# Performance work log

Measured on AMD Instinct MI355X. Metric: run time of the kernel, lower is better.

The kernel has to match this reference:

```python
import jax, jax.numpy as jnp
import numpy as np

N, E, IN, H, OUT, K = 50000, 800000, 128, 128, 40, 10
ALPHA, EPS, AH = 0.1, 1e-5, 64


def setup_inputs() -> dict:
    key = jax.random.key(0)
    ks = jax.random.split(key, 32)
    rn = lambda k, s, sc=0.05: jax.random.normal(k, s, jnp.float32) * sc
    return dict(
        x=jax.random.normal(ks[0], (N, IN), jnp.float32),
        edge_index=jax.random.randint(ks[1], (2, E), 0, N, jnp.int64),
        edge_weight=jax.random.uniform(ks[2], (E,), jnp.float32),
        lin1_w=rn(ks[3], (H, IN)), lin1_b=rn(ks[4], (H,)),
        bn1_g=jnp.ones((H,), jnp.float32), bn1_b=jnp.zeros((H,), jnp.float32),
        bn1_m=rn(ks[5], (H,)), bn1_v=jax.random.uniform(ks[6], (H,), jnp.float32, 0.5, 1.5),
        lin2_w=rn(ks[7], (H, H)), lin2_b=rn(ks[8], (H,)),
        bn2_g=jnp.ones((H,), jnp.float32), bn2_b=jnp.zeros((H,), jnp.float32),
        bn2_m=rn(ks[9], (H,)), bn2_v=jax.random.uniform(ks[10], (H,), jnp.float32, 0.5, 1.5),
        att1_w=rn(ks[11], (AH, 2 * H)), att1_b=rn(ks[12], (AH,)),
        att2_w=rn(ks[13], (K + 1, AH)), att2_b=rn(ks[14], (K + 1,)),
        head1_w=rn(ks[15], (H // 2, H)), head1_b=rn(ks[16], (H // 2,)),
        bn3_g=jnp.ones((H // 2,), jnp.float32), bn3_b=jnp.zeros((H // 2,), jnp.float32),
        bn3_m=rn(ks[17], (H // 2,)), bn3_v=jax.random.uniform(ks[18], (H // 2,), jnp.float32, 0.5, 1.5),
        head2_w=rn(ks[19], (OUT, H // 2)), head2_b=rn(ks[20], (OUT,)),
    )


def _bn(x, g, b, m, v):
    # eval-mode BatchNorm1d with running stats
    return (x - m) * jax.lax.rsqrt(v + EPS) * g + b


def reference(x, edge_index, edge_weight,
              lin1_w, lin1_b, bn1_g, bn1_b, bn1_m, bn1_v,
              lin2_w, lin2_b, bn2_g, bn2_b, bn2_m, bn2_v,
              att1_w, att1_b, att2_w, att2_b,
              head1_w, head1_b, bn3_g, bn3_b, bn3_m, bn3_v,
              head2_w, head2_b):
    row, col = edge_index[0], edge_index[1]

    # dense stem (dropout is identity in eval mode)
    h = jax.nn.relu(_bn(x @ lin1_w.T + lin1_b, bn1_g, bn1_b, bn1_m, bn1_v))
    identity = h
    h = jax.nn.relu(_bn(h @ lin2_w.T + lin2_b, bn2_g, bn2_b, bn2_m, bn2_v)) + identity
    base = h  # h0 for APPNP

    # edge normalization (loop-invariant): w_e / clamp(sum_w(row), 1)
    wsum = jnp.clip(jax.ops.segment_sum(edge_weight, row, num_segments=N), 1.0)
    enorm = edge_weight / wsum[row]  # [E]

    xs = [h]
    for _ in range(K):  # fixed K iterations of gather -> scatter-add
        agg = jax.ops.segment_sum(h[row] * enorm[:, None], col, num_segments=N)
        h = (1.0 - ALPHA) * agg + ALPHA * base
        xs.append(h)

    stacked = jnp.stack(xs, axis=-1)                    # [N, H, K+1]
    ctx = jnp.concatenate([xs[0], xs[-1]], axis=-1)     # [N, 2H]
    a = jax.nn.gelu(ctx @ att1_w.T + att1_b, approximate=False) @ att2_w.T + att2_b
    w = jax.nn.softmax(a, axis=-1)[:, None, :]          # [N, 1, K+1]
    fused = (stacked * w).sum(axis=-1)                  # [N, H]

    z = jax.nn.relu(_bn(fused @ head1_w.T + head1_b, bn3_g, bn3_b, bn3_m, bn3_v))
    return z @ head2_w.T + head2_b
```

## Files before the change

### kernel.cpp

```cpp
#include <hip/hip_runtime.h>
#include <hip/hip_fp16.h>
#include <math.h>

#define NN 50000
#define EE 800000
#define HH 128
#define KIT 10
#define NHF (NN * HH)
#define CC 64
#define CH 12500
#define RRH 4
#define NRH 12500

typedef _Float16 half8 __attribute__((ext_vector_type(8)));
typedef _Float16 half4v __attribute__((ext_vector_type(4)));
typedef float floatx4 __attribute__((ext_vector_type(4)));

static_assert(NN % 16 == 0, "row tiles must be exact");

__device__ __forceinline__ float gelu_exact(float x) {
  return 0.5f * x * (1.f + erff(x * 0.70710678118654752f));
}

__device__ __forceinline__ float4 ld4(const float* p) { return *(const float4*)p; }
__device__ __forceinline__ float4 ld4(const __half* p) {
  const __half2* q = (const __half2*)p;
  float2 lo = __half22float2(q[0]);
  float2 hi = __half22float2(q[1]);
  return make_float4(lo.x, lo.y, hi.x, hi.y);
}
__device__ __forceinline__ void st1(float* p, float v) { *p = v; }
__device__ __forceinline__ void st1(__half* p, float v) { *p = __float2half_rn(v); }

__global__ __launch_bounds__(256) void hist2_kernel(const int* __restrict__ ei,
                                                    const float* __restrict__ ew,
                                                    int* __restrict__ pdeg,
                                                    float* __restrict__ pwsum,
                                                    int* __restrict__ rank) {
  __shared__ int hist[NRH];
  const int c = blockIdx.x;
  const int z = blockIdx.y;
  const bool isdeg = (z < RRH);
  const int lo = (isdeg ? z : z - RRH) * NRH;
  for (int i = threadIdx.x; i < NRH; i += 256) hist[i] = 0;
  __syncthreads();
  const int e0 = c * CH;
  if (isdeg) {
    const int4* d4 = (const int4*)(ei + (size_t)EE + e0);
    for (int i = threadIdx.x; i < CH / 4; i += 256) {
      int4 d = d4[i];
      int e = e0 + i * 4;
      unsigned u0 = (unsigned)(d.x - lo), u1 = (unsigned)(d.y - lo);
      unsigned u2 = (unsigned)(d.z - lo), u3 = (unsigned)(d.w - lo);
      if (u0 < NRH) rank[e]     = atomicAdd(&hist[u0], 1);
      if (u1 < NRH) rank[e + 1] = atomicAdd(&hist[u1], 1);
      if (u2 < NRH) rank[e + 2] = atomicAdd(&hist[u2], 1);
      if (u3 < NRH) rank[e + 3] = atomicAdd(&hist[u3], 1);
    }
    __syncthreads();
    for (int i = threadIdx.x; i < NRH; i += 256)
      pdeg[(size_t)c * NN + lo + i] = hist[i];
  } else {
    float* whist = (float*)hist;
    const int4* s4 = (const int4*)(ei + e0);
    const float4* w4 = (const float4*)(ew + e0);
    for (int i = threadIdx.x; i < CH / 4; i += 256) {
      int4 s = s4[i];
      float4 w = w4[i];
      unsigned u0 = (unsigned)(s.x - lo), u1 = (unsigned)(s.y - lo);
      unsigned u2 = (unsigned)(s.z - lo), u3 = (unsigned)(s.w - lo);
      if (u0 < NRH) atomicAdd(&whist[u0], w.x);
      if (u1 < NRH) atomicAdd(&whist[u1], w.y);
      if (u2 < NRH) atomicAdd(&whist[u2], w.z);
      if (u3 < NRH) atomicAdd(&whist[u3], w.w);
    }
    __syncthreads();
    for (int i = threadIdx.x; i < NRH; i += 256)
      pwsum[(size_t)c * NN + lo + i] = whist[i];
  }
}

__global__ __launch_bounds__(256) void reduce_kernel(int* __restrict__ pdeg,
                                                     const float* __restrict__ pwsum,
                                                     int* __restrict__ deg,
                                                     float* __restrict__ wsum,
                                                     int* __restrict__ bsum) {
  int node = blockIdx.x * 256 + threadIdx.x;
  int acc = 0; float wacc = 0.f;
  if (node < NN) {
    for (int c = 0; c < CC; ++c) {
      size_t idx = (size_t)c * NN + node;
      int t = pdeg[idx];
      pdeg[idx] = acc;
      acc += t;
      wacc += pwsum[idx];
    }
    deg[node] = acc;
    wsum[node] = wacc;
  }
  __shared__ int red[256];
  red[threadIdx.x] = (node < NN) ? ((acc + 7) & ~7) : 0;
  __syncthreads();
  for (int off = 128; off > 0; off >>= 1) {
    if (threadIdx.x < off) red[threadIdx.x] += red[threadIdx.x + off];
    __syncthreads();
  }
  if (threadIdx.x == 0) bsum[blockIdx.x] = red[0];
}

__global__ __launch_bounds__(256) void scan2_kernel(const int* __restrict__ bsum,
                                                    int* __restrict__ boff,
                                                    int* __restrict__ row_start, int nb, int n) {
  __shared__ int buf[256];
  int tid = threadIdx.x;
  int v = (tid < nb) ? bsum[tid] : 0;
  buf[tid] = v;
  __syncthreads();
  for (int off = 1; off < 256; off <<= 1) {
    int t = (tid >= off) ? buf[tid - off] : 0;
    __syncthreads();
    buf[tid] += t;
    __syncthreads();
  }
  if (tid < nb) boff[tid] = buf[tid] - v;
  if (tid == 255) row_start[n] = buf[255];
}

__global__ __launch_bounds__(256) void scan3_kernel(const int* __restrict__ deg,
                                                    const int* __restrict__ boff,
                                                    int* __restrict__ row_start, int n) {
  __shared__ int buf[256];
  int tid = threadIdx.x;
  int i = blockIdx.x * 256 + tid;
  int v = (i < n) ? ((deg[i] + 7) & ~7) : 0;
  buf[tid] = v;
  __syncthreads();
  for (int off = 1; off < 256; off <<= 1) {
    int t = (tid >= off) ? buf[tid - off] : 0;
    __syncthreads();
    buf[tid] += t;
    __syncthreads();
  }
  if (i < n) row_start[i] = boff[blockIdx.x] + buf[tid] - v;
}

__global__ __launch_bounds__(256) void csr_fill_kernel(const int* __restrict__ ei,
                                                       const float* __restrict__ ew,
                                                       const float* __restrict__ wsum,
                                                       const int* __restrict__ row_start,
                                                       const int* __restrict__ pdeg_excl,
                                                       const int* __restrict__ rank,
                                                       int2* __restrict__ csr, int e_cnt) {
  int e = blockIdx.x * 256 + threadIdx.x;
  if (e >= e_cnt) return;
  int c = e / CH;
  int src = ei[e], dst = ei[EE + e];
  float ws = wsum[src];
  ws = ws < 1.f ? 1.f : ws;
  float v = 0.9f * ew[e] / ws;
  int pos = row_start[dst] + pdeg_excl[(size_t)c * NN + dst] + rank[e];
  csr[pos] = make_int2(src, __float_as_int(v));
}

__global__ __launch_bounds__(256) void pad_fill_kernel(const int* __restrict__ deg,
                                                       const int* __restrict__ row_start,
                                                       long* __restrict__ csr) {
  int node = blockIdx.x * 256 + threadIdx.x;
  if (node >= NN) return;
  int s = row_start[node] + deg[node];
  int e = row_start[node + 1];
  for (int i = s; i < e; ++i) csr[i] = 0;
}

__global__ __launch_bounds__(256, 6) void prop_kernel(const __half* __restrict__ h_cur,
                                                      const __half* __restrict__ base,
                                                      const int* __restrict__ row_start,
                                                      const long* __restrict__ csr,
                                                      __half* __restrict__ h_next) {
  int pair = __builtin_amdgcn_readfirstlane((int)blockIdx.x * 4 + (int)(threadIdx.x >> 6));
  int nA = pair * 2;
  if (nA >= NN) return;
  int nB = nA + 1;
  int lane = threadIdx.x & 63;
  const __half2* hc = (const __half2*)h_cur;
  float2 vbA = __half22float2(((const __half2*)base)[(size_t)nA * 64 + lane]);
  float2 vbB = __half22float2(((const __half2*)base)[(size_t)nB * 64 + lane]);
  float aAx = 0.1f * vbA.x, aAy = 0.1f * vbA.y, bAx = 0.f, bAy = 0.f;
  float aBx = 0.1f * vbB.x, aBy = 0.1f * vbB.y, bBx = 0.f, bBy = 0.f;
  int s  = __builtin_amdgcn_readfirstlane(row_start[nA]);
  int eA = __builtin_amdgcn_readfirstlane(row_start[nA + 1]);
  int eB = __builtin_amdgcn_readfirstlane(row_start[nB + 1]);
  int nb = (eB - s) >> 3;
  int i = s;
  if (nb > 0) {
    long cur[8];
    bool curB = (i >= eA);
#pragma unroll
    for (int j = 0; j < 8; ++j) cur[j] = csr[i + j];
    i += 8;
    for (int bidx = 1; bidx < nb; ++bidx) {
      long nxt[8];
      bool nxtB = (i >= eA);
#pragma unroll
      for (int j = 0; j < 8; ++j) nxt[j] = csr[i + j];
      i += 8;
      float2 g[8];
#pragma unroll
      for (int j = 0; j < 8; ++j) g[j] = __half22float2(hc[(size_t)(int)cur[j] * 64 + lane]);
      if (curB) {
#pragma unroll
        for (int j = 0; j < 8; ++j) {
          float v = __int_as_float((int)(cur[j] >> 32));
          if (j & 1) { bBx = fmaf(v, g[j].x, bBx); bBy = fmaf(v, g[j].y, bBy); }
          else       { aBx = fmaf(v, g[j].x, aBx); aBy = fmaf(v, g[j].y, aBy); }
        }
      } else {
#pragma unroll
        for (int j = 0; j < 8; ++j) {
          float v = __int_as_float((int)(cur[j] >> 32));
          if (j & 1) { bAx = fmaf(v, g[j].x, bAx); bAy = fmaf(v, g[j].y, bAy); }
          else       { aAx = fmaf(v, g[j].x, aAx); aAy = fmaf(v, g[j].y, aAy); }
        }
      }
#pragma unroll
      for (int j = 0; j < 8; ++j) cur[j] = nxt[j];
      curB = nxtB;
    }
    float2 g[8];
#pragma unroll
    for (int j = 0; j < 8; ++j) g[j] = __half22float2(hc[(size_t)(int)cur[j] * 64 + lane]);
    if (curB) {
#pragma unroll
      for (int j = 0; j < 8; ++j) {
        float v = __int_as_float((int)(cur[j] >> 32));
        if (j & 1) { bBx = fmaf(v, g[j].x, bBx); bBy = fmaf(v, g[j].y, bBy); }
        else       { aBx = fmaf(v, g[j].x, aBx); aBy = fmaf(v, g[j].y, aBy); }
      }
    } else {
#pragma unroll
      for (int j = 0; j < 8; ++j) {
        float v = __int_as_float((int)(cur[j] >> 32));
        if (j & 1) { bAx = fmaf(v, g[j].x, bAx); bAy = fmaf(v, g[j].y, bAy); }
        else       { aAx = fmaf(v, g[j].x, aAx); aAy = fmaf(v, g[j].y, aAy); }
      }
    }
  }
  ((__half2*)h_next)[(size_t)nA * 64 + lane] =
      __float22half2_rn(make_float2(aAx + bAx, aAy + bAy));
  ((__half2*)h_next)[(size_t)nB * 64 + lane] =
      __float22half2_rn(make_float2(aBx + bBx, aBy + bBy));
}

template <int K, int KA, int JP, int JR, int ACT, bool RESID, typename IT, typename OT>
__global__ __launch_bounds__(256) void mfma_dense2(
    const IT* __restrict__ Xa, const IT* __restrict__ Xb,
    const float* __restrict__ W, const float* __restrict__ lb,
    const float* __restrict__ bg, const float* __restrict__ bb,
    const float* __restrict__ bm, const float* __restrict__ bv,
    const OT* __restrict__ resid, OT* __restrict__ out) {
  static_assert(K % 32 == 0 && KA % 32 == 0 && JP % 16 == 0, "");
  constexpr int JT = JP / 16;
  constexpr int NS = K / 32;
  constexpr bool ISF = __is_same(IT, float);
  __shared__ _Float16 wL[JP][K];

  const int tid = threadIdx.x;
  const int wv = tid >> 6, lane = tid & 63;
  const int q = lane >> 4, m = lane & 15;
  const int t = blockIdx.x * 4 + wv;
  const bool active = (t < NN / 16);
  const int row = t * 16 + m;

  half8  a[ISF ? 1 : NS];
  float4 af0[ISF ? NS : 1], af1[ISF ? NS : 1];
  if (active) {
#pragma unroll
    for (int s = 0; s < NS; ++s) {
      int c = s * 32 + q * 8;
      if constexpr (ISF) {
        const float* p = (const float*)Xa + (size_t)row * K + c;
        af0[s] = *(const float4*)p;
        af1[s] = *(const float4*)(p + 4);
      } else {
        const __half* p = (c < KA) ? (const __half*)Xa + (size_t)row * KA + c
                                   : (const __half*)Xb + (size_t)row * (K - KA) + (c - KA);
        a[s] = *(const half8*)p;
      }
    }
  }

  constexpr int C4 = K / 4;
  for (int idx = tid; idx < JP * C4; idx += 256) {
    int j = idx / C4;
    int c4 = (idx % C4) * 4;
    float4 v = make_float4(0.f, 0.f, 0.f, 0.f);
    if (j < JR) v = *(const float4*)&W[(size_t)j * K + c4];
    int cs = ((((c4 >> 3) ^ (j & 7)) << 3) | (c4 & 7));
    *(half4v*)&wL[j][cs] = (half4v){(_Float16)v.x, (_Float16)v.y,
                                    (_Float16)v.z, (_Float16)v.w};
  }
  __syncthreads();

  if (!active) return;

  floatx4 acc[JT];
#pragma unroll
  for (int jt = 0; jt < JT; ++jt) acc[jt] = (floatx4)(0.f);

#pragma unroll
  for (int s = 0; s < NS; ++s) {
    half8 av;
    if constexpr (ISF) {
      float4 f0 = af0[s], f1 = af1[s];
      av = (half8){(_Float16)f0.x, (_Float16)f0.y, (_Float16)f0.z, (_Float16)f0.w,
                   (_Float16)f1.x, (_Float16)f1.y, (_Float16)f1.z, (_Float16)f1.w};
    } else {
      av = a[s];
    }
    int kq = s * 4 + q;
#pragma unroll
    for (int jt = 0; jt < JT; ++jt) {
      int j = jt * 16 + m;
      half8 b = *(const half8*)&wL[j][(kq ^ (j & 7)) << 3];
      acc[jt] = __builtin_amdgcn_mfma_f32_16x16x32_f16(av, b, acc[jt], 0, 0, 0);
    }
  }

#pragma unroll
  for (int jt = 0; jt < JT; ++jt) {
    int j = jt * 16 + m;
    if (j >= JR) continue;
    float sc = 0.f, sh;
    if (ACT == 1) {
      sc = bg[j] * rsqrtf(bv[j] + 1e-5f);
      sh = (lb[j] - bm[j]) * sc + bb[j];
    } else {
      sh = lb[j];
    }
#pragma unroll
    for (int reg = 0; reg < 4; ++reg) {
      int r = t * 16 + q * 4 + reg;
      float aa = acc[jt][reg];
      float y;
      if (ACT == 0)      y = aa + sh;
      else if (ACT == 1) y = fmaxf(fmaf(aa, sc, sh), 0.f);
      else               y = gelu_exact(aa + sh);
      if (RESID) y += (float)resid[(size_t)r * JR + j];
      st1(&out[(size_t)r * JR + j], y);
    }
  }
}

__global__ __launch_bounds__(64) void att2_softmax_kernel(const __half* __restrict__ g,
                                                          const float* __restrict__ W2,
                                                          const float* __restrict__ b2,
                                                          float* __restrict__ attw, int n_rows) {
  __shared__ float gl[64][65];
  int r0 = blockIdx.x * 64;
  for (int idx = threadIdx.x; idx < 64 * 16; idx += 64) {
    int r = idx >> 4, c4 = (idx & 15) * 4;
    float4 v = make_float4(0.f, 0.f, 0.f, 0.f);
    if (r0 + r < n_rows) v = ld4(&g[(size_t)(r0 + r) * 64 + c4]);
    gl[r][c4] = v.x; gl[r][c4 + 1] = v.y; gl[r][c4 + 2] = v.z; gl[r][c4 + 3] = v.w;
  }
  __syncthreads();
  int r = threadIdx.x;
  int n = r0 + r;
  if (n >= n_rows) return;
  float a[KIT + 1];
#pragma unroll
  for (int j = 0; j < KIT + 1; ++j) {
    float acc = b2[j];
#pragma unroll
    for (int k = 0; k < 64; ++k) acc = fmaf(gl[r][k], W2[j * 64 + k], acc);
    a[j] = acc;
  }
  float mx = a[0];
#pragma unroll
  for (int j = 1; j < KIT + 1; ++j) mx = fmaxf(mx, a[j]);
  float s = 0.f;
#pragma unroll
  for (int j = 0; j < KIT + 1; ++j) { a[j] = expf(a[j] - mx); s += a[j]; }
  float inv = 1.f / s;
#pragma unroll
  for (int j = 0; j < KIT + 1; ++j) attw[n * 16 + j] = a[j] * inv;
}

__global__ __launch_bounds__(256) void fused_gather_kernel(const __half* __restrict__ XS,
                                                           const float* __restrict__ attw,
                                                           __half* __restrict__ fused) {
  int node = __builtin_amdgcn_readfirstlane((int)blockIdx.x * 4 + (int)(threadIdx.x >> 6));
  if (node >= NN) return;
  int lane = threadIdx.x & 63;
  float ax = 0.f, ay = 0.f;
#pragma unroll
  for (int k = 0; k <= KIT; ++k) {
    float wk = attw[node * 16 + k];
    float2 v = __half22float2(((const __half2*)(XS + (size_t)k * NHF))[(size_t)node * 64 + lane]);
    ax = fmaf(wk, v.x, ax);
    ay = fmaf(wk, v.y, ay);
  }
  ((__half2*)fused)[(size_t)node * 64 + lane] = __float22half2_rn(make_float2(ax, ay));
}

__global__ __launch_bounds__(256) void fused_accum_kernel(const __half* __restrict__ h,
                                                          const float* __restrict__ attw,
                                                          float* __restrict__ fused, int k) {
  int node = __builtin_amdgcn_readfirstlane((int)blockIdx.x * 4 + (int)(threadIdx.x >> 6));
  if (node >= NN) return;
  int lane = threadIdx.x & 63;
  float wk = attw[node * 16 + k];
  float2 v = __half22float2(((const __half2*)h)[(size_t)node * 64 + lane]);
  float2 o;
  if (k == 0) {
    o = make_float2(wk * v.x, wk * v.y);
  } else {
    float2 f = ((const float2*)fused)[(size_t)node * 64 + lane];
    o = make_float2(fmaf(wk, v.x, f.x), fmaf(wk, v.y, f.y));
  }
  ((float2*)fused)[(size_t)node * 64 + lane] = o;
}

extern "C" void kernel_launch(void* const* d_in, const int* in_sizes, int n_in,
                              void* d_out, int out_size, void* d_ws, size_t ws_size,
                              hipStream_t stream) {
  (void)in_sizes; (void)n_in; (void)out_size;
  const float* x      = (const float*)d_in[0];
  const int*   ei     = (const int*)d_in[1];
  const float* ew     = (const float*)d_in[2];
  const float* lin1_w = (const float*)d_in[3];
  const float* lin1_b = (const float*)d_in[4];
  const float* bn1_g  = (const float*)d_in[5];
  const float* bn1_b  = (const float*)d_in[6];
  const float* bn1_m  = (const float*)d_in[7];
  const float* bn1_v  = (const float*)d_in[8];
  const float* lin2_w = (const float*)d_in[9];
  const float* lin2_b = (const float*)d_in[10];
  const float* bn2_g  = (const float*)d_in[11];
  const float* bn2_b  = (const float*)d_in[12];
  const float* bn2_m  = (const float*)d_in[13];
  const float* bn2_v  = (const float*)d_in[14];
  const float* att1_w = (const float*)d_in[15];
  const float* att1_b = (const float*)d_in[16];
  const float* att2_w = (const float*)d_in[17];
  const float* att2_b = (const float*)d_in[18];
  const float* head1_w= (const float*)d_in[19];
  const float* head1_b= (const float*)d_in[20];
  const float* bn3_g  = (const float*)d_in[21];
  const float* bn3_b  = (const float*)d_in[22];
  const float* bn3_m  = (const float*)d_in[23];
  const float* bn3_v  = (const float*)d_in[24];
  const float* head2_w= (const float*)d_in[25];
  const float* head2_b= (const float*)d_in[26];
  float* out = (float*)d_out;

  char* p = (char*)d_ws;
  auto alloc = [&](size_t bytes) -> void* {
    void* r = (void*)p;
    p += (bytes + 255) & ~(size_t)255;
    return r;
  };
  int*   row_start= (int*)alloc((size_t)(NN + 1) * 4);
  int*   bsum     = (int*)alloc((size_t)256 * 4);
  int*   boff     = (int*)alloc((size_t)256 * 4);
  int*   deg      = (int*)alloc((size_t)NN * 4);
  float* wsum     = (float*)alloc((size_t)NN * 4);
  long*  csr      = (long*)alloc(((size_t)EE + 8 * NN) * 8);
  __half* gbuf    = (__half*)alloc((size_t)NN * 64 * 2);
  float* attw     = (float*)alloc((size_t)NN * 16 * 4);
  __half* h1      = (__half*)alloc((size_t)NHF * 2);
  __half* fusedH  = (__half*)alloc((size_t)NHF * 2);
  __half* zbuf    = (__half*)alloc((size_t)NN * 64 * 2);
  size_t common = (size_t)(p - (char*)d_ws);
  size_t stored_need = common + (size_t)(KIT + 1) * NHF * 2 + 4096;
  bool stored = ws_size >= stored_need;

  __half* XS = nullptr;
  int* pdeg; float* pwsum; int* rank;
  if (stored) {
    XS = (__half*)alloc((size_t)(KIT + 1) * NHF * 2);
    char* ovl = (char*)(XS + (size_t)8 * NHF);
    pdeg  = (int*)ovl;
    pwsum = (float*)(ovl + (size_t)CC * NN * 4);
    rank  = (int*)(ovl + 2 * (size_t)CC * NN * 4);
  } else {
    pdeg  = (int*)alloc((size_t)CC * NN * 4);
    pwsum = (float*)alloc((size_t)CC * NN * 4);
    rank  = (int*)alloc((size_t)EE * 4);
  }

  const int GE  = (EE + 255) / 256;
  const int GN  = (NN + 255) / 256;
  const int GT  = (NN / 16 + 3) / 4;
  const int GP  = (NN + 3) / 4;
  const int GP2 = (NN / 2 + 3) / 4;
  const int GA  = (NN + 63) / 64;

  hist2_kernel<<<dim3(CC, 2 * RRH), 256, 0, stream>>>(ei, ew, pdeg, pwsum, rank);
  reduce_kernel<<<GN, 256, 0, stream>>>(pdeg, pwsum, deg, wsum, bsum);
  scan2_kernel<<<1, 256, 0, stream>>>(bsum, boff, row_start, GN, NN);
  scan3_kernel<<<GN, 256, 0, stream>>>(deg, boff, row_start, NN);
  csr_fill_kernel<<<GE, 256, 0, stream>>>(ei, ew, wsum, row_start, pdeg, rank,
                                          (int2*)csr, EE);
  pad_fill_kernel<<<GN, 256, 0, stream>>>(deg, row_start, csr);

  if (stored) {
    mfma_dense2<128, 128, 128, 128, 1, false, float, __half><<<GT, 256, 0, stream>>>(
        x, (const float*)nullptr, lin1_w, lin1_b, bn1_g, bn1_b, bn1_m, bn1_v, nullptr, h1);
    mfma_dense2<128, 128, 128, 128, 1, true, __half, __half><<<GT, 256, 0, stream>>>(
        h1, (const __half*)nullptr, lin2_w, lin2_b, bn2_g, bn2_b, bn2_m, bn2_v, h1, XS);
    for (int k = 0; k < KIT; ++k) {
      prop_kernel<<<GP2, 256, 0, stream>>>(XS + (size_t)k * NHF, XS, row_start,
                                           csr, XS + (size_t)(k + 1) * NHF);
    }
    mfma_dense2<256, 128, 64, 64, 2, false, __half, __half><<<GT, 256, 0, stream>>>(
        XS, XS + (size_t)KIT * NHF, att1_w, att1_b, nullptr, nullptr, nullptr, nullptr,
        nullptr, gbuf);
    att2_softmax_kernel<<<GA, 64, 0, stream>>>(gbuf, att2_w, att2_b, attw, NN);
    fused_gather_kernel<<<GP, 256, 0, stream>>>(XS, attw, fusedH);
    mfma_dense2<128, 128, 64, 64, 1, false, __half, __half><<<GT, 256, 0, stream>>>(
        fusedH, (const __half*)nullptr, head1_w, head1_b, bn3_g, bn3_b, bn3_m, bn3_v,
        nullptr, zbuf);
  } else {
    float*  fusedF = (float*)alloc((size_t)NHF * 4);
    __half* base   = (__half*)alloc((size_t)NHF * 2);
    __half* hA     = (__half*)alloc((size_t)NHF * 2);
    __half* hB     = (__half*)alloc((size_t)NHF * 2);
    mfma_dense2<128, 128, 128, 128, 1, false, float, __half><<<GT, 256, 0, stream>>>(
        x, (const float*)nullptr, lin1_w, lin1_b, bn1_g, bn1_b, bn1_m, bn1_v, nullptr, h1);
    mfma_dense2<128, 128, 128, 128, 1, true, __half, __half><<<GT, 256, 0, stream>>>(
        h1, (const __half*)nullptr, lin2_w, lin2_b, bn2_g, bn2_b, bn2_m, bn2_v, h1, base);
    const __half* cur = base;
    for (int k = 1; k <= KIT; ++k) {
      __half* nxt = (k & 1) ? hA : hB;
      prop_kernel<<<GP2, 256, 0, stream>>>(cur, base, row_start, csr, nxt);
      cur = nxt;
    }
    mfma_dense2<256, 128, 64, 64, 2, false, __half, __half><<<GT, 256, 0, stream>>>(
        base, cur, att1_w, att1_b, nullptr, nullptr, nullptr, nullptr, nullptr, gbuf);
    att2_softmax_kernel<<<GA, 64, 0, stream>>>(gbuf, att2_w, att2_b, attw, NN);
    fused_accum_kernel<<<GP, 256, 0, stream>>>(base, attw, fusedF, 0);
    cur = base;
    for (int k = 1; k <= KIT; ++k) {
      __half* nxt = (k & 1) ? hA : hB;
      prop_kernel<<<GP2, 256, 0, stream>>>(cur, base, row_start, csr, nxt);
      fused_accum_kernel<<<GP, 256, 0, stream>>>(nxt, attw, fusedF, k);
      cur = nxt;
    }
    mfma_dense2<128, 128, 64, 64, 1, false, float, __half><<<GT, 256, 0, stream>>>(
        fusedF, (const float*)nullptr, head1_w, head1_b, bn3_g, bn3_b, bn3_m, bn3_v,
        nullptr, zbuf);
  }

  mfma_dense2<64, 64, 48, 40, 0, false, __half, float><<<GT, 256, 0, stream>>>(
      zbuf, (const __half*)nullptr, head2_w, head2_b, nullptr, nullptr, nullptr, nullptr,
      nullptr, out);
}
```

Before: 564.9 us.

## Fuse propagation iterations into persistent kernel with grid barrier; fold attention gather into head GEMM

Replaces the ten separate propagation launches with one persistent kernel of 1024 blocks that loops over iterations and synchronises through a hierarchical atomic grid barrier in global memory. The barrier counters are zeroed in the pad-fill kernel. It also removes the separate fused-gather kernel and the fusedH buffer by computing the attention-weighted sum of the 11 stored hidden states inside the head1 MFMA kernel's A-operand load. This targets launch gaps and one extra write and read of an N×H buffer. The risks are deadlock if the 1024 blocks are not all co-resident, lower occupancy from the fixed grid, and the spin-wait cost at each barrier.

```diff
diff --git a/kernel.cpp b/kernel.cpp
--- a/kernel.cpp
+++ b/kernel.cpp
@@ -11,6 +11,7 @@
 #define CH 12500
 #define RRH 4
 #define NRH 12500
+#define GFUSE 1024
 
 typedef _Float16 half8 __attribute__((ext_vector_type(8)));
 typedef _Float16 half4v __attribute__((ext_vector_type(4)));
@@ -164,7 +165,9 @@
 
 __global__ __launch_bounds__(256) void pad_fill_kernel(const int* __restrict__ deg,
                                                        const int* __restrict__ row_start,
-                                                       long* __restrict__ csr) {
+                                                       long* __restrict__ csr,
+                                                       int* __restrict__ bar) {
+  if (blockIdx.x == 0 && threadIdx.x < 128) bar[threadIdx.x] = 0;
   int node = blockIdx.x * 256 + threadIdx.x;
   if (node >= NN) return;
   int s = row_start[node] + deg[node];
@@ -172,19 +175,15 @@
   for (int i = s; i < e; ++i) csr[i] = 0;
 }
 
-__global__ __launch_bounds__(256, 6) void prop_kernel(const __half* __restrict__ h_cur,
-                                                      const __half* __restrict__ base,
-                                                      const int* __restrict__ row_start,
-                                                      const long* __restrict__ csr,
-                                                      __half* __restrict__ h_next) {
-  int pair = __builtin_amdgcn_readfirstlane((int)blockIdx.x * 4 + (int)(threadIdx.x >> 6));
-  int nA = pair * 2;
-  if (nA >= NN) return;
+__device__ __forceinline__ void prop_pair(int nA, int lane,
+                                          const __half2* __restrict__ hc,
+                                          const __half2* __restrict__ bp,
+                                          const int* __restrict__ row_start,
+                                          const long* __restrict__ csr,
+                                          __half2* __restrict__ np) {
   int nB = nA + 1;
-  int lane = threadIdx.x & 63;
-  const __half2* hc = (const __half2*)h_cur;
-  float2 vbA = __half22float2(((const __half2*)base)[(size_t)nA * 64 + lane]);
-  float2 vbB = __half22float2(((const __half2*)base)[(size_t)nB * 64 + lane]);
+  float2 vbA = __half22float2(bp[(size_t)nA * 64 + lane]);
+  float2 vbB = __half22float2(bp[(size_t)nB * 64 + lane]);
   float aAx = 0.1f * vbA.x, aAy = 0.1f * vbA.y, bAx = 0.f, bAy = 0.f;
   float aBx = 0.1f * vbB.x, aBy = 0.1f * vbB.y, bBx = 0.f, bBy = 0.f;
   int s  = __builtin_amdgcn_readfirstlane(row_start[nA]);
@@ -245,19 +244,69 @@
       }
     }
   }
-  ((__half2*)h_next)[(size_t)nA * 64 + lane] =
-      __float22half2_rn(make_float2(aAx + bAx, aAy + bAy));
-  ((__half2*)h_next)[(size_t)nB * 64 + lane] =
-      __float22half2_rn(make_float2(aBx + bBx, aBy + bBy));
-}
-
-template <int K, int KA, int JP, int JR, int ACT, bool RESID, typename IT, typename OT>
+  np[(size_t)nA * 64 + lane] = __float22half2_rn(make_float2(aAx + bAx, aAy + bAy));
+  np[(size_t)nB * 64 + lane] = __float22half2_rn(make_float2(aBx + bBx, aBy + bBy));
+}
+
+__global__ __launch_bounds__(256, 6) void prop_kernel(const __half* __restrict__ h_cur,
+                                                      const __half* __restrict__ base,
+                                                      const int* __restrict__ row_start,
+                                                      const long* __restrict__ csr,
+                                                      __half* __restrict__ h_next) {
+  int pair = __builtin_amdgcn_readfirstlane((int)blockIdx.x * 4 + (int)(threadIdx.x >> 6));
+  if (pair * 2 >= NN) return;
+  prop_pair(pair * 2, threadIdx.x & 63, (const __half2*)h_cur, (const __half2*)base,
+            row_start, csr, (__half2*)h_next);
+}
+
+__global__ __launch_bounds__(256, 4) void prop_fused_kernel(__half* XS,
+                                                            const int* __restrict__ row_start,
+                                                            const long* __restrict__ csr,
+                                                            int* bar, int niter) {
+  const int TOTW = GFUSE * 4;
+  const int wid = (int)blockIdx.x * 4 + (int)(threadIdx.x >> 6);
+  const int lane = threadIdx.x & 63;
+  const __half2* bp = (const __half2*)XS;
+  for (int k = 0; k < niter; ++k) {
+    const __half2* hcp = (const __half2*)(XS + (size_t)k * NHF);
+    __half2* npp = (__half2*)(XS + (size_t)(k + 1) * NHF);
+    for (int pr = wid; pr < NN / 2; pr += TOTW)
+      prop_pair(pr * 2, lane, hcp, bp, row_start, csr, npp);
+    if (k == niter - 1) break;
+    __syncthreads();
+    if (threadIdx.x == 0) {
+      __threadfence();
+      int s = (int)blockIdx.x & 63;
+      int v = __hip_atomic_fetch_add(&bar[s], 1, __ATOMIC_ACQ_REL,
+                                     __HIP_MEMORY_SCOPE_AGENT);
+      if (v == (GFUSE / 64) - 1) {
+        __hip_atomic_store(&bar[s], 0, __ATOMIC_RELAXED, __HIP_MEMORY_SCOPE_AGENT);
+        int m = __hip_atomic_fetch_add(&bar[64], 1, __ATOMIC_ACQ_REL,
+                                       __HIP_MEMORY_SCOPE_AGENT);
+        if (m == 63) {
+          __hip_atomic_store(&bar[64], 0, __ATOMIC_RELAXED, __HIP_MEMORY_SCOPE_AGENT);
+          __hip_atomic_store(&bar[65], k + 1, __ATOMIC_RELEASE,
+                             __HIP_MEMORY_SCOPE_AGENT);
+        }
+      }
+      while (__hip_atomic_load(&bar[65], __ATOMIC_ACQUIRE,
+                               __HIP_MEMORY_SCOPE_AGENT) < k + 1)
+        __builtin_amdgcn_s_sleep(2);
+      __threadfence();
+    }
+    __syncthreads();
+  }
+}
+
+template <int K, int KA, int JP, int JR, int ACT, bool RESID, typename IT, typename OT,
+          bool FG = false>
 __global__ __launch_bounds__(256) void mfma_dense2(
     const IT* __restrict__ Xa, const IT* __restrict__ Xb,
     const float* __restrict__ W, const float* __restrict__ lb,
     const float* __restrict__ bg, const float* __restrict__ bb,
     const float* __restrict__ bm, const float* __restrict__ bv,
-    const OT* __restrict__ resid, OT* __restrict__ out) {
+    const OT* __restrict__ resid, OT* __restrict__ out,
+    const float* __restrict__ attwp = nullptr) {
   static_assert(K % 32 == 0 && KA % 32 == 0 && JP % 16 == 0, "");
   constexpr int JT = JP / 16;
   constexpr int NS = K / 32;
@@ -273,18 +322,25 @@
 
   half8  a[ISF ? 1 : NS];
   float4 af0[ISF ? NS : 1], af1[ISF ? NS : 1];
+  float awr[FG ? 12 : 1];
   if (active) {
-#pragma unroll
-    for (int s = 0; s < NS; ++s) {
-      int c = s * 32 + q * 8;
-      if constexpr (ISF) {
-        const float* p = (const float*)Xa + (size_t)row * K + c;
-        af0[s] = *(const float4*)p;
-        af1[s] = *(const float4*)(p + 4);
-      } else {
-        const __half* p = (c < KA) ? (const __half*)Xa + (size_t)row * KA + c
-                                   : (const __half*)Xb + (size_t)row * (K - KA) + (c - KA);
-        a[s] = *(const half8*)p;
+    if constexpr (FG) {
+      *(float4*)&awr[0] = *(const float4*)&attwp[row * 16 + 0];
+      *(float4*)&awr[4] = *(const float4*)&attwp[row * 16 + 4];
+      *(float4*)&awr[8] = *(const float4*)&attwp[row * 16 + 8];
+    } else {
+#pragma unroll
+      for (int s = 0; s < NS; ++s) {
+        int c = s * 32 + q * 8;
+        if constexpr (ISF) {
+          const float* p = (const float*)Xa + (size_t)row * K + c;
+          af0[s] = *(const float4*)p;
+          af1[s] = *(const float4*)(p + 4);
+        } else {
+          const __half* p = (c < KA) ? (const __half*)Xa + (size_t)row * KA + c
+                                     : (const __half*)Xb + (size_t)row * (K - KA) + (c - KA);
+          a[s] = *(const half8*)p;
+        }
       }
     }
   }
@@ -310,7 +366,18 @@
 #pragma unroll
   for (int s = 0; s < NS; ++s) {
     half8 av;
-    if constexpr (ISF) {
+    if constexpr (FG) {
+      float f[8] = {0.f, 0.f, 0.f, 0.f, 0.f, 0.f, 0.f, 0.f};
+      const __half* bptr = (const __half*)Xa + (size_t)row * K + (s * 32 + q * 8);
+#pragma unroll
+      for (int k = 0; k <= KIT; ++k) {
+        half8 v = *(const half8*)(bptr + (size_t)k * NHF);
+#pragma unroll
+        for (int e = 0; e < 8; ++e) f[e] = fmaf(awr[k], (float)v[e], f[e]);
+      }
+      av = (half8){(_Float16)f[0], (_Float16)f[1], (_Float16)f[2], (_Float16)f[3],
+                   (_Float16)f[4], (_Float16)f[5], (_Float16)f[6], (_Float16)f[7]};
+    } else if constexpr (ISF) {
       float4 f0 = af0[s], f1 = af1[s];
       av = (half8){(_Float16)f0.x, (_Float16)f0.y, (_Float16)f0.z, (_Float16)f0.w,
                    (_Float16)f1.x, (_Float16)f1.y, (_Float16)f1.z, (_Float16)f1.w};
@@ -384,23 +451,6 @@
   float inv = 1.f / s;
 #pragma unroll
   for (int j = 0; j < KIT + 1; ++j) attw[n * 16 + j] = a[j] * inv;
-}
-
-__global__ __launch_bounds__(256) void fused_gather_kernel(const __half* __restrict__ XS,
-                                                           const float* __restrict__ attw,
-                                                           __half* __restrict__ fused) {
-  int node = __builtin_amdgcn_readfirstlane((int)blockIdx.x * 4 + (int)(threadIdx.x >> 6));
-  if (node >= NN) return;
-  int lane = threadIdx.x & 63;
-  float ax = 0.f, ay = 0.f;
-#pragma unroll
-  for (int k = 0; k <= KIT; ++k) {
-    float wk = attw[node * 16 + k];
-    float2 v = __half22float2(((const __half2*)(XS + (size_t)k * NHF))[(size_t)node * 64 + lane]);
-    ax = fmaf(wk, v.x, ax);
-    ay = fmaf(wk, v.y, ay);
-  }
-  ((__half2*)fused)[(size_t)node * 64 + lane] = __float22half2_rn(make_float2(ax, ay));
 }
 
 __global__ __launch_bounds__(256) void fused_accum_kernel(const __half* __restrict__ h,
@@ -463,13 +513,13 @@
   int*   row_start= (int*)alloc((size_t)(NN + 1) * 4);
   int*   bsum     = (int*)alloc((size_t)256 * 4);
   int*   boff     = (int*)alloc((size_t)256 * 4);
+  int*   bar      = (int*)alloc((size_t)256 * 4);
   int*   deg      = (int*)alloc((size_t)NN * 4);
   float* wsum     = (float*)alloc((size_t)NN * 4);
   long*  csr      = (long*)alloc(((size_t)EE + 8 * NN) * 8);
   __half* gbuf    = (__half*)alloc((size_t)NN * 64 * 2);
   float* attw     = (float*)alloc((size_t)NN * 16 * 4);
   __half* h1      = (__half*)alloc((size_t)NHF * 2);
-  __half* fusedH  = (__half*)alloc((size_t)NHF * 2);
   __half* zbuf    = (__half*)alloc((size_t)NN * 64 * 2);
   size_t common = (size_t)(p - (char*)d_ws);
   size_t stored_need = common + (size_t)(KIT + 1) * NHF * 2 + 4096;
@@ -502,25 +552,21 @@
   scan3_kernel<<<GN, 256, 0, stream>>>(deg, boff, row_start, NN);
   csr_fill_kernel<<<GE, 256, 0, stream>>>(ei, ew, wsum, row_start, pdeg, rank,
                                           (int2*)csr, EE);
-  pad_fill_kernel<<<GN, 256, 0, stream>>>(deg, row_start, csr);
+  pad_fill_kernel<<<GN, 256, 0, stream>>>(deg, row_start, csr, bar);
 
   if (stored) {
     mfma_dense2<128, 128, 128, 128, 1, false, float, __half><<<GT, 256, 0, stream>>>(
         x, (const float*)nullptr, lin1_w, lin1_b, bn1_g, bn1_b, bn1_m, bn1_v, nullptr, h1);
     mfma_dense2<128, 128, 128, 128, 1, true, __half, __half><<<GT, 256, 0, stream>>>(
         h1, (const __half*)nullptr, lin2_w, lin2_b, bn2_g, bn2_b, bn2_m, bn2_v, h1, XS);
-    for (int k = 0; k < KIT; ++k) {
-      prop_kernel<<<GP2, 256, 0, stream>>>(XS + (size_t)k * NHF, XS, row_start,
-                                           csr, XS + (size_t)(k + 1) * NHF);
-    }
+    prop_fused_kernel<<<GFUSE, 256, 0, stream>>>(XS, row_start, csr, bar, KIT);
     mfma_dense2<256, 128, 64, 64, 2, false, __half, __half><<<GT, 256, 0, stream>>>(
         XS, XS + (size_t)KIT * NHF, att1_w, att1_b, nullptr, nullptr, nullptr, nullptr,
         nullptr, gbuf);
     att2_softmax_kernel<<<GA, 64, 0, stream>>>(gbuf, att2_w, att2_b, attw, NN);
-    fused_gather_kernel<<<GP, 256, 0, stream>>>(XS, attw, fusedH);
-    mfma_dense2<128, 128, 64, 64, 1, false, __half, __half><<<GT, 256, 0, stream>>>(
-        fusedH, (const __half*)nullptr, head1_w, head1_b, bn3_g, bn3_b, bn3_m, bn3_v,
-        nullptr, zbuf);
+    mfma_dense2<128, 128, 64, 64, 1, false, __half, __half, true><<<GT, 256, 0, stream>>>(
+        XS, (const __half*)nullptr, head1_w, head1_b, bn3_g, bn3_b, bn3_m, bn3_v,
+        nullptr, zbuf, attw);
   } else {
     float*  fusedF = (float*)alloc((size_t)NHF * 4);
     __half* base   = (__half*)alloc((size_t)NHF * 2);
```

Result: slower. 1.942 ms (+243.8%).
